# Optimization experiments

Measured on AMD Instinct MI355X. Metric: run time of the kernel, lower is better.

## Reference

```python
import jax, jax.numpy as jnp
import numpy as np

NUM_USERS = 100000
NUM_RATINGS = 5
EMBED_DIM = 64
ATT_DIM = 16
B, G, L, S = 16384, 8, 50, 32


def setup_inputs() -> dict:
    key = jax.random.key(0)
    ks = jax.random.split(key, 16)
    inp = {
        # forward args (int / bool constants)
        "nodes": jax.random.randint(ks[0], (B, G), 0, NUM_USERS),
        "history_u": jax.random.randint(ks[1], (B, L), 0, NUM_USERS),
        "history_r": jax.random.randint(ks[2], (B, L), 0, NUM_RATINGS),
        "history_mask": jax.random.randint(ks[3], (B, L), 0, 2).astype(bool).at[:, 0].set(True),
        "social_adj": jax.random.randint(ks[4], (B, S), 0, NUM_USERS),
        "social_mask": jax.random.randint(ks[5], (B, S), 0, 2).astype(bool).at[:, 0].set(True),
        # learned parameters
        "features": jax.random.normal(ks[6], (NUM_USERS, EMBED_DIM), jnp.float32) * 0.02,
        "r_embed": jax.random.normal(ks[7], (NUM_RATINGS, EMBED_DIM), jnp.float32) * 0.02,
        "wg1": jax.random.normal(ks[8], (EMBED_DIM, ATT_DIM), jnp.float32) / np.sqrt(EMBED_DIM),
        "bg1": jnp.zeros((ATT_DIM,), jnp.float32),
        "wg2": jax.random.normal(ks[9], (ATT_DIM, 1), jnp.float32) / np.sqrt(ATT_DIM),
        "bg2": jnp.zeros((1,), jnp.float32),
        "w1": jax.random.normal(ks[10], (2 * EMBED_DIM, EMBED_DIM), jnp.float32) / np.sqrt(2 * EMBED_DIM),
        "b1": jnp.zeros((EMBED_DIM,), jnp.float32),
    }
    return inp


def _masked_mean(x, mask):
    # x: [B, N, D], mask: [B, N] float -> [B, D]
    denom = jnp.maximum(mask.sum(axis=1, keepdims=True), 1.0)
    return (x * mask[..., None]).sum(axis=1) / denom


def reference(nodes, history_u, history_r, history_mask, social_adj, social_mask,
              features, r_embed, wg1, bg1, wg2, bg2, w1, b1):
    dt = features.dtype
    # --- Group_Embedding: attention pooling over member embeddings ---
    members = features[nodes]                              # [B, G, D] gather
    h = jnp.tanh(members @ wg1 + bg1)                      # [B, G, 16]
    logits = (h @ wg2 + bg2)[..., 0]                       # [B, G]
    alpha = jax.nn.softmax(logits, axis=-1)
    self_feats = jnp.einsum('bg,bgd->bd', alpha, members)  # [B, D]

    # --- aggregator: ragged history (item+rating) + social neighbor means ---
    hm = history_mask.astype(dt)
    hist = features[history_u] + r_embed[history_r]        # [B, L, D] gather
    hist_mean = _masked_mean(hist, hm)                     # [B, D]

    sm = social_mask.astype(dt)
    soc_mean = _masked_mean(features[social_adj], sm)      # [B, D]

    neigh_feats = 0.5 * (hist_mean + soc_mean)             # [B, D]

    # --- concat -> linear -> relu ---
    combined = jnp.concatenate([self_feats, neigh_feats], axis=1)  # [B, 2D]
    return jax.nn.relu(combined @ w1 + b1)                 # [B, D]
```

## Files before the change

kernel.cpp:

```cpp
#include <hip/hip_runtime.h>
#include <cstdint>
#include <cstddef>

#define NUSERS 100000
#define BB 16384

static __device__ __forceinline__ unsigned short f2bf(float x) {
    unsigned u = __float_as_uint(x);
    u += 0x7FFF + ((u >> 16) & 1);
    return (unsigned short)(u >> 16);
}
static __device__ __forceinline__ float4 bf4_to_f4(ushort4 h) {
    float4 r;
    r.x = __uint_as_float((unsigned)h.x << 16);
    r.y = __uint_as_float((unsigned)h.y << 16);
    r.z = __uint_as_float((unsigned)h.z << 16);
    r.w = __uint_as_float((unsigned)h.w << 16);
    return r;
}

__global__ __launch_bounds__(256) void k0_scores(
    const float* __restrict__ features, const float* __restrict__ wg1,
    const float* __restrict__ bg1, const float* __restrict__ wg2,
    const float* __restrict__ bg2, float* __restrict__ Q,
    unsigned short* __restrict__ fbf)
{
    __shared__ float frow[16 * 68];
    __shared__ float wg1t[16 * 68];
    const int tid = threadIdx.x;
    const int blk = blockIdx.x;

    const float4 v = ((const float4*)(features + (size_t)blk * 1024))[tid];
    {
        const int row = tid >> 4, q = tid & 15;
        *(float4*)&frow[row * 68 + q * 4] = v;
    }
    {
        const float4 w = ((const float4*)wg1)[tid];
        const int d = tid >> 2, k0 = (tid & 3) * 4;
        wg1t[(k0 + 0) * 68 + d] = w.x;
        wg1t[(k0 + 1) * 68 + d] = w.y;
        wg1t[(k0 + 2) * 68 + d] = w.z;
        wg1t[(k0 + 3) * 68 + d] = w.w;
    }
    {
        ushort4 o;
        o.x = f2bf(v.x); o.y = f2bf(v.y); o.z = f2bf(v.z); o.w = f2bf(v.w);
        *(ushort4*)(fbf + (size_t)blk * 1024 + tid * 4) = o;
    }
    __syncthreads();

    const int k = tid & 15, ul = tid >> 4;
    float x = bg1[k];
    #pragma unroll
    for (int d4 = 0; d4 < 16; ++d4) {
        const float4 f  = *(const float4*)&frow[ul * 68 + d4 * 4];
        const float4 wv = *(const float4*)&wg1t[k * 68 + d4 * 4];
        x += f.x * wv.x + f.y * wv.y + f.z * wv.z + f.w * wv.w;
    }
    float xx = fminf(fmaxf(x, -9.f), 9.f);
    float e2 = __expf(2.f * xx);
    float th = (e2 - 1.f) / (e2 + 1.f);
    float t = th * wg2[k];
    t += __shfl_xor(t, 1);
    t += __shfl_xor(t, 2);
    t += __shfl_xor(t, 4);
    t += __shfl_xor(t, 8);
    if (k == 0) Q[blk * 16 + ul] = t + bg2[0];
}

__global__ __launch_bounds__(256) void k1_fuse(
    const int* __restrict__ nodes, const int* __restrict__ hist_u,
    const int* __restrict__ hist_r, const int* __restrict__ hist_m,
    const int* __restrict__ soc_a, const int* __restrict__ soc_m,
    const unsigned short* __restrict__ fbf, const float* __restrict__ r_embed,
    const float* __restrict__ Q, const float* __restrict__ w1,
    const float* __restrict__ b1, float* __restrict__ out)
{
    __shared__ float wvbuf[4][128];

    const int tid  = threadIdx.x;
    const int lane = tid & 63;
    const int wv   = tid >> 6;
    const int e    = blockIdx.x * 4 + wv;
    const int sub  = lane & 15;
    const int grp  = lane >> 4;
    const char* fb = (const char*)fbf;

    int*   lc = (int*)&wvbuf[wv][0];
    float* cb = &wvbuf[wv][0];

    lc[lane] = 0;
    if (lane < 32) lc[64 + lane] = 0;

    int nd = (lane < 8) ? nodes[e * 8 + lane] : 0;
    int hu = 0, hr = 0, hmv = 0;
    if (lane < 50) {
        hu  = hist_u[e * 50 + lane];
        hr  = hist_r[e * 50 + lane];
        hmv = hist_m[e * 50 + lane];
    }
    int sa = 0, sk = 0;
    if (lane < 32) {
        sa = soc_a[e * 32 + lane];
        sk = soc_m[e * 32 + lane];
    }

    uint64_t hb = __ballot(hmv != 0);
    const int hc = (int)__popcll(hb);
    int hrank = (int)__popcll(hb & ((1ull << lane) - 1));

    uint64_t sbm = __ballot(sk != 0);
    const int scn = (int)__popcll(sbm);
    int srank = (int)__popcll(sbm & ((1ull << lane) - 1));

    const float hw = 0.5f / (float)hc;
    const float sw = 0.5f / (float)scn;
    const int   n  = hc + scn;

    if (hmv) lc[hrank] = hu << 7;
    if (sk)  lc[hc + srank] = sa << 7;

    const int c0 = (int)__popcll(__ballot(hmv && hr == 0));
    const int c1 = (int)__popcll(__ballot(hmv && hr == 1));
    const int c2 = (int)__popcll(__ballot(hmv && hr == 2));
    const int c3 = (int)__popcll(__ballot(hmv && hr == 3));
    const int c4 = (int)__popcll(__ballot(hmv && hr == 4));

    int pkA = lc[lane];
    int pkB = lc[64 + (lane & 31)];

    float sc = (lane < 8) ? Q[nd] : -1e30f;
    float mx = sc;
    mx = fmaxf(mx, __shfl_xor(mx, 1));
    mx = fmaxf(mx, __shfl_xor(mx, 2));
    mx = fmaxf(mx, __shfl_xor(mx, 4));
    float ex = __expf(sc - mx);
    float sm = ex;
    sm += __shfl_xor(sm, 1);
    sm += __shfl_xor(sm, 2);
    sm += __shfl_xor(sm, 4);
    float al = ex / sm;

    float4 sf4;
    {
        const float a0 = __shfl(al, grp);
        const int   u0 = __shfl(nd, grp);
        const float a1 = __shfl(al, 4 + grp);
        const int   u1 = __shfl(nd, 4 + grp);
        const float4 v0 = bf4_to_f4(*(const ushort4*)(fb + ((unsigned)u0 << 7) + sub * 8));
        const float4 v1 = bf4_to_f4(*(const ushort4*)(fb + ((unsigned)u1 << 7) + sub * 8));
        sf4.x = a0 * v0.x + a1 * v1.x;
        sf4.y = a0 * v0.y + a1 * v1.y;
        sf4.z = a0 * v0.z + a1 * v1.z;
        sf4.w = a0 * v0.w + a1 * v1.w;
    }

    float4 nb4 = {0.f, 0.f, 0.f, 0.f};
    for (int base = 0; base < n; base += 16) {
        #pragma unroll
        for (int j = 0; j < 4; ++j) {
            const int cbase = base + j * 4;
            int off;
            if (cbase < 64) off = __shfl(pkA, cbase + grp);
            else            off = __shfl(pkB, cbase - 64 + grp);
            const int idx = cbase + grp;
            const float w = (idx < hc) ? hw : ((idx < n) ? sw : 0.f);
            const float4 v = bf4_to_f4(*(const ushort4*)(fb + (unsigned)off + sub * 8));
            nb4.x += w * v.x; nb4.y += w * v.y;
            nb4.z += w * v.z; nb4.w += w * v.w;
        }
    }

#define XRED(v4)                                            \
    v4.x += __shfl_xor(v4.x, 16); v4.x += __shfl_xor(v4.x, 32); \
    v4.y += __shfl_xor(v4.y, 16); v4.y += __shfl_xor(v4.y, 32); \
    v4.z += __shfl_xor(v4.z, 16); v4.z += __shfl_xor(v4.z, 32); \
    v4.w += __shfl_xor(v4.w, 16); v4.w += __shfl_xor(v4.w, 32);
    XRED(sf4)
    XRED(nb4)
#undef XRED

    {
        const float4* re4p = (const float4*)r_embed;
        const float4 re0 = re4p[0 * 16 + sub];
        const float4 re1 = re4p[1 * 16 + sub];
        const float4 re2 = re4p[2 * 16 + sub];
        const float4 re3 = re4p[3 * 16 + sub];
        const float4 re4 = re4p[4 * 16 + sub];
        float f0 = hw * (float)c0, f1 = hw * (float)c1, f2 = hw * (float)c2,
              f3 = hw * (float)c3, f4 = hw * (float)c4;
        nb4.x += f0 * re0.x + f1 * re1.x + f2 * re2.x + f3 * re3.x + f4 * re4.x;
        nb4.y += f0 * re0.y + f1 * re1.y + f2 * re2.y + f3 * re3.y + f4 * re4.y;
        nb4.z += f0 * re0.z + f1 * re1.z + f2 * re2.z + f3 * re3.z + f4 * re4.z;
        nb4.w += f0 * re0.w + f1 * re1.w + f2 * re2.w + f3 * re3.w + f4 * re4.w;
    }

    if (grp == 0) *(float4*)&cb[sub * 4] = sf4;
    if (grp == 1) *(float4*)&cb[64 + sub * 4] = nb4;

    float4 p = {0.f, 0.f, 0.f, 0.f};
    #pragma unroll 8
    for (int j = 0; j < 32; ++j) {
        const float  c   = cb[j * 4 + grp];
        const float4 wv4 = *(const float4*)(w1 + (j * 4 + grp) * 64 + sub * 4);
        p.x += c * wv4.x;
        p.y += c * wv4.y;
        p.z += c * wv4.z;
        p.w += c * wv4.w;
    }
    p.x += __shfl_xor(p.x, 16); p.x += __shfl_xor(p.x, 32);
    p.y += __shfl_xor(p.y, 16); p.y += __shfl_xor(p.y, 32);
    p.z += __shfl_xor(p.z, 16); p.z += __shfl_xor(p.z, 32);
    p.w += __shfl_xor(p.w, 16); p.w += __shfl_xor(p.w, 32);
    if (grp == 0) {
        const float4 bv = *(const float4*)(b1 + sub * 4);
        float4 o;
        o.x = fmaxf(p.x + bv.x, 0.f);
        o.y = fmaxf(p.y + bv.y, 0.f);
        o.z = fmaxf(p.z + bv.z, 0.f);
        o.w = fmaxf(p.w + bv.w, 0.f);
        *(float4*)(out + (size_t)e * 64 + sub * 4) = o;
    }
}

extern "C" void kernel_launch(void* const* d_in, const int* in_sizes, int n_in,
                              void* d_out, int out_size, void* d_ws, size_t ws_size,
                              hipStream_t stream)
{
    const int*   nodes    = (const int*)d_in[0];
    const int*   hu       = (const int*)d_in[1];
    const int*   hr       = (const int*)d_in[2];
    const int*   hm       = (const int*)d_in[3];
    const int*   sa       = (const int*)d_in[4];
    const int*   smk      = (const int*)d_in[5];
    const float* features = (const float*)d_in[6];
    const float* r_embed  = (const float*)d_in[7];
    const float* wg1      = (const float*)d_in[8];
    const float* bg1      = (const float*)d_in[9];
    const float* wg2      = (const float*)d_in[10];
    const float* bg2      = (const float*)d_in[11];
    const float* w1       = (const float*)d_in[12];
    const float* b1       = (const float*)d_in[13];
    float* out = (float*)d_out;

    float*          Q   = (float*)d_ws;
    unsigned short* fbf = (unsigned short*)(Q + 131072);

    k0_scores<<<NUSERS / 16, 256, 0, stream>>>(features, wg1, bg1, wg2, bg2, Q, fbf);
    k1_fuse<<<BB / 4, 256, 0, stream>>>(nodes, hu, hr, hm, sa, smk,
                                        fbf, r_embed, Q, w1, b1, out);
}
```

Before: 138.5 us.

## Gather bf16 rows with 16-byte loads, 8 rows per wave per step

```diff
diff --git a/kernel.cpp b/kernel.cpp
--- a/kernel.cpp
+++ b/kernel.cpp
@@ -10,13 +10,16 @@
     u += 0x7FFF + ((u >> 16) & 1);
     return (unsigned short)(u >> 16);
 }
-static __device__ __forceinline__ float4 bf4_to_f4(ushort4 h) {
-    float4 r;
-    r.x = __uint_as_float((unsigned)h.x << 16);
-    r.y = __uint_as_float((unsigned)h.y << 16);
-    r.z = __uint_as_float((unsigned)h.z << 16);
-    r.w = __uint_as_float((unsigned)h.w << 16);
-    return r;
+
+static __device__ __forceinline__ void acc8(float* acc, uint4 q, float w) {
+    acc[0] += w * __uint_as_float(q.x << 16);
+    acc[1] += w * __uint_as_float(q.x & 0xffff0000u);
+    acc[2] += w * __uint_as_float(q.y << 16);
+    acc[3] += w * __uint_as_float(q.y & 0xffff0000u);
+    acc[4] += w * __uint_as_float(q.z << 16);
+    acc[5] += w * __uint_as_float(q.z & 0xffff0000u);
+    acc[6] += w * __uint_as_float(q.w << 16);
+    acc[7] += w * __uint_as_float(q.w & 0xffff0000u);
 }
 
 __global__ __launch_bounds__(256) void k0_scores(
@@ -85,6 +88,8 @@
     const int e    = blockIdx.x * 4 + wv;
     const int sub  = lane & 15;
     const int grp  = lane >> 4;
+    const int oct  = lane >> 3;
+    const int s8   = lane & 7;
     const char* fb = (const char*)fbf;
 
     int*   lc = (int*)&wvbuf[wv][0];
@@ -131,6 +136,31 @@
     int pkB = lc[64 + (lane & 31)];
 
     float sc = (lane < 8) ? Q[nd] : -1e30f;
+    const int um = __shfl(nd, oct);
+    const uint4 mq = *(const uint4*)(fb + ((unsigned)um << 7) + s8 * 16);
+
+    float nb[8] = {0.f, 0.f, 0.f, 0.f, 0.f, 0.f, 0.f, 0.f};
+    for (int base = 0; base < n; base += 32) {
+        const int b0 = base, b1_ = base + 8, b2 = base + 16, b3 = base + 24;
+        const int off0 = (b0  < 64) ? __shfl(pkA, b0  + oct) : __shfl(pkB, b0  - 64 + oct);
+        const int off1 = (b1_ < 64) ? __shfl(pkA, b1_ + oct) : __shfl(pkB, b1_ - 64 + oct);
+        const int off2 = (b2  < 64) ? __shfl(pkA, b2  + oct) : __shfl(pkB, b2  - 64 + oct);
+        const int off3 = (b3  < 64) ? __shfl(pkA, b3  + oct) : __shfl(pkB, b3  - 64 + oct);
+        const uint4 q0 = *(const uint4*)(fb + (unsigned)off0 + s8 * 16);
+        const uint4 q1 = *(const uint4*)(fb + (unsigned)off1 + s8 * 16);
+        const uint4 q2 = *(const uint4*)(fb + (unsigned)off2 + s8 * 16);
+        const uint4 q3 = *(const uint4*)(fb + (unsigned)off3 + s8 * 16);
+        const int i0 = b0 + oct, i1 = b1_ + oct, i2 = b2 + oct, i3 = b3 + oct;
+        const float w0 = (i0 < hc) ? hw : ((i0 < n) ? sw : 0.f);
+        const float w1q= (i1 < hc) ? hw : ((i1 < n) ? sw : 0.f);
+        const float w2 = (i2 < hc) ? hw : ((i2 < n) ? sw : 0.f);
+        const float w3 = (i3 < hc) ? hw : ((i3 < n) ? sw : 0.f);
+        acc8(nb, q0, w0);
+        acc8(nb, q1, w1q);
+        acc8(nb, q2, w2);
+        acc8(nb, q3, w3);
+    }
+
     float mx = sc;
     mx = fmaxf(mx, __shfl_xor(mx, 1));
     mx = fmaxf(mx, __shfl_xor(mx, 2));
@@ -142,62 +172,47 @@
     sm += __shfl_xor(sm, 4);
     float al = ex / sm;
 
-    float4 sf4;
-    {
-        const float a0 = __shfl(al, grp);
-        const int   u0 = __shfl(nd, grp);
-        const float a1 = __shfl(al, 4 + grp);
-        const int   u1 = __shfl(nd, 4 + grp);
-        const float4 v0 = bf4_to_f4(*(const ushort4*)(fb + ((unsigned)u0 << 7) + sub * 8));
-        const float4 v1 = bf4_to_f4(*(const ushort4*)(fb + ((unsigned)u1 << 7) + sub * 8));
-        sf4.x = a0 * v0.x + a1 * v1.x;
-        sf4.y = a0 * v0.y + a1 * v1.y;
-        sf4.z = a0 * v0.z + a1 * v1.z;
-        sf4.w = a0 * v0.w + a1 * v1.w;
-    }
-
-    float4 nb4 = {0.f, 0.f, 0.f, 0.f};
-    for (int base = 0; base < n; base += 16) {
-        #pragma unroll
-        for (int j = 0; j < 4; ++j) {
-            const int cbase = base + j * 4;
-            int off;
-            if (cbase < 64) off = __shfl(pkA, cbase + grp);
-            else            off = __shfl(pkB, cbase - 64 + grp);
-            const int idx = cbase + grp;
-            const float w = (idx < hc) ? hw : ((idx < n) ? sw : 0.f);
-            const float4 v = bf4_to_f4(*(const ushort4*)(fb + (unsigned)off + sub * 8));
-            nb4.x += w * v.x; nb4.y += w * v.y;
-            nb4.z += w * v.z; nb4.w += w * v.w;
-        }
-    }
-
-#define XRED(v4)                                            \
-    v4.x += __shfl_xor(v4.x, 16); v4.x += __shfl_xor(v4.x, 32); \
-    v4.y += __shfl_xor(v4.y, 16); v4.y += __shfl_xor(v4.y, 32); \
-    v4.z += __shfl_xor(v4.z, 16); v4.z += __shfl_xor(v4.z, 32); \
-    v4.w += __shfl_xor(v4.w, 16); v4.w += __shfl_xor(v4.w, 32);
-    XRED(sf4)
-    XRED(nb4)
-#undef XRED
-
-    {
-        const float4* re4p = (const float4*)r_embed;
-        const float4 re0 = re4p[0 * 16 + sub];
-        const float4 re1 = re4p[1 * 16 + sub];
-        const float4 re2 = re4p[2 * 16 + sub];
-        const float4 re3 = re4p[3 * 16 + sub];
-        const float4 re4 = re4p[4 * 16 + sub];
-        float f0 = hw * (float)c0, f1 = hw * (float)c1, f2 = hw * (float)c2,
-              f3 = hw * (float)c3, f4 = hw * (float)c4;
-        nb4.x += f0 * re0.x + f1 * re1.x + f2 * re2.x + f3 * re3.x + f4 * re4.x;
-        nb4.y += f0 * re0.y + f1 * re1.y + f2 * re2.y + f3 * re3.y + f4 * re4.y;
-        nb4.z += f0 * re0.z + f1 * re1.z + f2 * re2.z + f3 * re3.z + f4 * re4.z;
-        nb4.w += f0 * re0.w + f1 * re1.w + f2 * re2.w + f3 * re3.w + f4 * re4.w;
-    }
-
-    if (grp == 0) *(float4*)&cb[sub * 4] = sf4;
-    if (grp == 1) *(float4*)&cb[64 + sub * 4] = nb4;
+    const float am = __shfl(al, oct);
+    float sf[8] = {0.f, 0.f, 0.f, 0.f, 0.f, 0.f, 0.f, 0.f};
+    acc8(sf, mq, am);
+
+    #pragma unroll
+    for (int k = 0; k < 8; ++k) {
+        nb[k] += __shfl_xor(nb[k], 8);
+        nb[k] += __shfl_xor(nb[k], 16);
+        nb[k] += __shfl_xor(nb[k], 32);
+        sf[k] += __shfl_xor(sf[k], 8);
+        sf[k] += __shfl_xor(sf[k], 16);
+        sf[k] += __shfl_xor(sf[k], 32);
+    }
+
+    {
+        const float4* r4 = (const float4*)r_embed;
+        const int qa = s8 * 2;
+        const float4 a0 = r4[0 * 16 + qa], b0 = r4[0 * 16 + qa + 1];
+        const float4 a1 = r4[1 * 16 + qa], b1v = r4[1 * 16 + qa + 1];
+        const float4 a2 = r4[2 * 16 + qa], b2v = r4[2 * 16 + qa + 1];
+        const float4 a3 = r4[3 * 16 + qa], b3v = r4[3 * 16 + qa + 1];
+        const float4 a4 = r4[4 * 16 + qa], b4v = r4[4 * 16 + qa + 1];
+        const float f0 = hw * (float)c0, f1 = hw * (float)c1, f2 = hw * (float)c2,
+                    f3 = hw * (float)c3, f4 = hw * (float)c4;
+        nb[0] += f0 * a0.x + f1 * a1.x + f2 * a2.x + f3 * a3.x + f4 * a4.x;
+        nb[1] += f0 * a0.y + f1 * a1.y + f2 * a2.y + f3 * a3.y + f4 * a4.y;
+        nb[2] += f0 * a0.z + f1 * a1.z + f2 * a2.z + f3 * a3.z + f4 * a4.z;
+        nb[3] += f0 * a0.w + f1 * a1.w + f2 * a2.w + f3 * a3.w + f4 * a4.w;
+        nb[4] += f0 * b0.x + f1 * b1v.x + f2 * b2v.x + f3 * b3v.x + f4 * b4v.x;
+        nb[5] += f0 * b0.y + f1 * b1v.y + f2 * b2v.y + f3 * b3v.y + f4 * b4v.y;
+        nb[6] += f0 * b0.z + f1 * b1v.z + f2 * b2v.z + f3 * b3v.z + f4 * b4v.z;
+        nb[7] += f0 * b0.w + f1 * b1v.w + f2 * b2v.w + f3 * b3v.w + f4 * b4v.w;
+    }
+
+    if (oct == 0) {
+        *(float4*)&cb[s8 * 8]     = make_float4(sf[0], sf[1], sf[2], sf[3]);
+        *(float4*)&cb[s8 * 8 + 4] = make_float4(sf[4], sf[5], sf[6], sf[7]);
+    } else if (oct == 1) {
+        *(float4*)&cb[64 + s8 * 8]     = make_float4(nb[0], nb[1], nb[2], nb[3]);
+        *(float4*)&cb[64 + s8 * 8 + 4] = make_float4(nb[4], nb[5], nb[6], nb[7]);
+    }
 
     float4 p = {0.f, 0.f, 0.f, 0.f};
     #pragma unroll 8
```

After: 140.6 us. No clear change (+1.5%).

## Precompute per-user W1 projections with MFMA and gather projected rows

Applied to the files above, without the earlier changes.

```diff
diff --git a/kernel.cpp b/kernel.cpp
--- a/kernel.cpp
+++ b/kernel.cpp
@@ -4,80 +4,146 @@
 
 #define NUSERS 100000
 #define BB 16384
+
+typedef __attribute__((ext_vector_type(8))) short bf16x8;
+typedef __attribute__((ext_vector_type(4))) float f32x4;
 
 static __device__ __forceinline__ unsigned short f2bf(float x) {
     unsigned u = __float_as_uint(x);
     u += 0x7FFF + ((u >> 16) & 1);
     return (unsigned short)(u >> 16);
 }
-static __device__ __forceinline__ float4 bf4_to_f4(ushort4 h) {
-    float4 r;
-    r.x = __uint_as_float((unsigned)h.x << 16);
-    r.y = __uint_as_float((unsigned)h.y << 16);
-    r.z = __uint_as_float((unsigned)h.z << 16);
-    r.w = __uint_as_float((unsigned)h.w << 16);
-    return r;
-}
-
-__global__ __launch_bounds__(256) void k0_scores(
-    const float* __restrict__ features, const float* __restrict__ wg1,
-    const float* __restrict__ bg1, const float* __restrict__ wg2,
-    const float* __restrict__ bg2, float* __restrict__ Q,
-    unsigned short* __restrict__ fbf)
+static __device__ __forceinline__ float bf2f(unsigned short h) {
+    return __uint_as_float((unsigned)h << 16);
+}
+
+__global__ __launch_bounds__(256) void k0_build(
+    const float* __restrict__ features, const float* __restrict__ r_embed,
+    const float* __restrict__ wg1, const float* __restrict__ bg1,
+    const float* __restrict__ wg2, const float* __restrict__ bg2,
+    const float* __restrict__ w1,
+    float* __restrict__ Q, float* __restrict__ RB, float* __restrict__ GH)
 {
-    __shared__ float frow[16 * 68];
-    __shared__ float wg1t[16 * 68];
+    __shared__ unsigned short Al[64 * 72];
+    __shared__ unsigned short Bt[128 * 72];
+    __shared__ float wg1t[16 * 72];
+
     const int tid = threadIdx.x;
     const int blk = blockIdx.x;
-
-    const float4 v = ((const float4*)(features + (size_t)blk * 1024))[tid];
-    {
-        const int row = tid >> 4, q = tid & 15;
-        *(float4*)&frow[row * 68 + q * 4] = v;
+    const int u0  = blk * 64;
+
+    #pragma unroll
+    for (int q = 0; q < 4; ++q) {
+        const int idx = tid + q * 256;
+        const int ul  = idx >> 4, qd = idx & 15;
+        float4 v = make_float4(0.f, 0.f, 0.f, 0.f);
+        if (u0 + ul < NUSERS)
+            v = *(const float4*)(features + (size_t)(u0 + ul) * 64 + qd * 4);
+        ushort4 o;
+        o.x = f2bf(v.x); o.y = f2bf(v.y); o.z = f2bf(v.z); o.w = f2bf(v.w);
+        *(ushort4*)&Al[ul * 72 + qd * 4] = o;
+    }
+    #pragma unroll
+    for (int q = 0; q < 8; ++q) {
+        const int idx = tid + q * 256;
+        const int r  = idx >> 4, cq = (idx & 15) * 4;
+        const float4 v = *(const float4*)(w1 + r * 64 + cq);
+        const int cc = (r < 64) ? cq : (64 + cq);
+        const int dd = (r < 64) ? r : (r - 64);
+        Bt[(cc + 0) * 72 + dd] = f2bf(v.x);
+        Bt[(cc + 1) * 72 + dd] = f2bf(v.y);
+        Bt[(cc + 2) * 72 + dd] = f2bf(v.z);
+        Bt[(cc + 3) * 72 + dd] = f2bf(v.w);
     }
     {
         const float4 w = ((const float4*)wg1)[tid];
-        const int d = tid >> 2, k0 = (tid & 3) * 4;
-        wg1t[(k0 + 0) * 68 + d] = w.x;
-        wg1t[(k0 + 1) * 68 + d] = w.y;
-        wg1t[(k0 + 2) * 68 + d] = w.z;
-        wg1t[(k0 + 3) * 68 + d] = w.w;
-    }
+        const int d = tid >> 2, k0q = (tid & 3) * 4;
+        wg1t[(k0q + 0) * 72 + d] = w.x;
+        wg1t[(k0q + 1) * 72 + d] = w.y;
+        wg1t[(k0q + 2) * 72 + d] = w.z;
+        wg1t[(k0q + 3) * 72 + d] = w.w;
+    }
+    __syncthreads();
+
+    const int lane = tid & 63, wv = tid >> 6;
+    const int arow = wv * 16 + (lane & 15);
+    const int hi   = lane >> 4;
+    f32x4 acc[8];
+    #pragma unroll
+    for (int ct = 0; ct < 8; ++ct) acc[ct] = (f32x4){0.f, 0.f, 0.f, 0.f};
+    #pragma unroll
+    for (int ks = 0; ks < 2; ++ks) {
+        const bf16x8 a = *(const bf16x8*)&Al[arow * 72 + ks * 32 + hi * 8];
+        #pragma unroll
+        for (int ct = 0; ct < 8; ++ct) {
+            const bf16x8 b = *(const bf16x8*)&Bt[(ct * 16 + (lane & 15)) * 72 + ks * 32 + hi * 8];
+            acc[ct] = __builtin_amdgcn_mfma_f32_16x16x32_bf16(a, b, acc[ct], 0, 0, 0);
+        }
+    }
+    #pragma unroll
+    for (int ct = 0; ct < 8; ++ct) {
+        #pragma unroll
+        for (int j = 0; j < 4; ++j) {
+            const int ul = wv * 16 + hi * 4 + j;
+            const int u  = u0 + ul;
+            if (u < NUSERS)
+                GH[(size_t)u * 128 + ct * 16 + (lane & 15)] = acc[ct][j];
+        }
+    }
+
     {
-        ushort4 o;
-        o.x = f2bf(v.x); o.y = f2bf(v.y); o.z = f2bf(v.z); o.w = f2bf(v.w);
-        *(ushort4*)(fbf + (size_t)blk * 1024 + tid * 4) = o;
-    }
-    __syncthreads();
-
-    const int k = tid & 15, ul = tid >> 4;
-    float x = bg1[k];
-    #pragma unroll
-    for (int d4 = 0; d4 < 16; ++d4) {
-        const float4 f  = *(const float4*)&frow[ul * 68 + d4 * 4];
-        const float4 wv = *(const float4*)&wg1t[k * 68 + d4 * 4];
-        x += f.x * wv.x + f.y * wv.y + f.z * wv.z + f.w * wv.w;
-    }
-    float xx = fminf(fmaxf(x, -9.f), 9.f);
-    float e2 = __expf(2.f * xx);
-    float th = (e2 - 1.f) / (e2 + 1.f);
-    float t = th * wg2[k];
-    t += __shfl_xor(t, 1);
-    t += __shfl_xor(t, 2);
-    t += __shfl_xor(t, 4);
-    t += __shfl_xor(t, 8);
-    if (k == 0) Q[blk * 16 + ul] = t + bg2[0];
+        const int k = tid & 15, ug = tid >> 4;
+        const float bg1v = bg1[k], wk2 = wg2[k], bg2v = bg2[0];
+        #pragma unroll
+        for (int un = 0; un < 4; ++un) {
+            const int ul = ug + un * 16;
+            float x = bg1v;
+            #pragma unroll
+            for (int d8 = 0; d8 < 8; ++d8) {
+                const ushort4 pa = *(const ushort4*)&Al[ul * 72 + d8 * 8];
+                const ushort4 pb = *(const ushort4*)&Al[ul * 72 + d8 * 8 + 4];
+                x += bf2f(pa.x) * wg1t[k * 72 + d8 * 8 + 0]
+                   + bf2f(pa.y) * wg1t[k * 72 + d8 * 8 + 1]
+                   + bf2f(pa.z) * wg1t[k * 72 + d8 * 8 + 2]
+                   + bf2f(pa.w) * wg1t[k * 72 + d8 * 8 + 3]
+                   + bf2f(pb.x) * wg1t[k * 72 + d8 * 8 + 4]
+                   + bf2f(pb.y) * wg1t[k * 72 + d8 * 8 + 5]
+                   + bf2f(pb.z) * wg1t[k * 72 + d8 * 8 + 6]
+                   + bf2f(pb.w) * wg1t[k * 72 + d8 * 8 + 7];
+            }
+            float xx = fminf(fmaxf(x, -9.f), 9.f);
+            float e2 = __expf(2.f * xx);
+            float th = (e2 - 1.f) / (e2 + 1.f);
+            float t = th * wk2;
+            t += __shfl_xor(t, 1);
+            t += __shfl_xor(t, 2);
+            t += __shfl_xor(t, 4);
+            t += __shfl_xor(t, 8);
+            if (k == 0 && u0 + ul < NUSERS) Q[u0 + ul] = t + bg2v;
+        }
+    }
+
+    if (blk == 0) {
+        for (int t = tid; t < 320; t += 256) {
+            const int r = t >> 6, c = t & 63;
+            float a = 0.f;
+            #pragma unroll 8
+            for (int d = 0; d < 64; ++d)
+                a += r_embed[r * 64 + d] * w1[(64 + d) * 64 + c];
+            RB[r * 64 + c] = a;
+        }
+    }
 }
 
 __global__ __launch_bounds__(256) void k1_fuse(
     const int* __restrict__ nodes, const int* __restrict__ hist_u,
     const int* __restrict__ hist_r, const int* __restrict__ hist_m,
     const int* __restrict__ soc_a, const int* __restrict__ soc_m,
-    const unsigned short* __restrict__ fbf, const float* __restrict__ r_embed,
-    const float* __restrict__ Q, const float* __restrict__ w1,
-    const float* __restrict__ b1, float* __restrict__ out)
+    const float* __restrict__ GH, const float* __restrict__ RB,
+    const float* __restrict__ Q, const float* __restrict__ b1,
+    float* __restrict__ out)
 {
-    __shared__ float wvbuf[4][128];
+    __shared__ int lcomp[4][96];
 
     const int tid  = threadIdx.x;
     const int lane = tid & 63;
@@ -85,10 +151,9 @@
     const int e    = blockIdx.x * 4 + wv;
     const int sub  = lane & 15;
     const int grp  = lane >> 4;
-    const char* fb = (const char*)fbf;
-
-    int*   lc = (int*)&wvbuf[wv][0];
-    float* cb = &wvbuf[wv][0];
+    const char* fb = (const char*)GH;
+
+    int* lc = lcomp[wv];
 
     lc[lane] = 0;
     if (lane < 32) lc[64 + lane] = 0;
@@ -118,8 +183,8 @@
     const float sw = 0.5f / (float)scn;
     const int   n  = hc + scn;
 
-    if (hmv) lc[hrank] = hu << 7;
-    if (sk)  lc[hc + srank] = sa << 7;
+    if (hmv) lc[hrank] = (hu << 9) + 256;
+    if (sk)  lc[hc + srank] = (sa << 9) + 256;
 
     const int c0 = (int)__popcll(__ballot(hmv && hr == 0));
     const int c1 = (int)__popcll(__ballot(hmv && hr == 1));
@@ -148,8 +213,8 @@
         const int   u0 = __shfl(nd, grp);
         const float a1 = __shfl(al, 4 + grp);
         const int   u1 = __shfl(nd, 4 + grp);
-        const float4 v0 = bf4_to_f4(*(const ushort4*)(fb + ((unsigned)u0 << 7) + sub * 8));
-        const float4 v1 = bf4_to_f4(*(const ushort4*)(fb + ((unsigned)u1 << 7) + sub * 8));
+        const float4 v0 = *(const float4*)(fb + ((unsigned)u0 << 9) + sub * 16);
+        const float4 v1 = *(const float4*)(fb + ((unsigned)u1 << 9) + sub * 16);
         sf4.x = a0 * v0.x + a1 * v1.x;
         sf4.y = a0 * v0.y + a1 * v1.y;
         sf4.z = a0 * v0.z + a1 * v1.z;
@@ -166,7 +231,7 @@
             else            off = __shfl(pkB, cbase - 64 + grp);
             const int idx = cbase + grp;
             const float w = (idx < hc) ? hw : ((idx < n) ? sw : 0.f);
-            const float4 v = bf4_to_f4(*(const ushort4*)(fb + (unsigned)off + sub * 8));
+            const float4 v = *(const float4*)(fb + (unsigned)off + sub * 16);
             nb4.x += w * v.x; nb4.y += w * v.y;
             nb4.z += w * v.z; nb4.w += w * v.w;
         }
@@ -182,44 +247,27 @@
 #undef XRED
 
     {
-        const float4* re4p = (const float4*)r_embed;
-        const float4 re0 = re4p[0 * 16 + sub];
-        const float4 re1 = re4p[1 * 16 + sub];
-        const float4 re2 = re4p[2 * 16 + sub];
-        const float4 re3 = re4p[3 * 16 + sub];
-        const float4 re4 = re4p[4 * 16 + sub];
-        float f0 = hw * (float)c0, f1 = hw * (float)c1, f2 = hw * (float)c2,
-              f3 = hw * (float)c3, f4 = hw * (float)c4;
-        nb4.x += f0 * re0.x + f1 * re1.x + f2 * re2.x + f3 * re3.x + f4 * re4.x;
-        nb4.y += f0 * re0.y + f1 * re1.y + f2 * re2.y + f3 * re3.y + f4 * re4.y;
-        nb4.z += f0 * re0.z + f1 * re1.z + f2 * re2.z + f3 * re3.z + f4 * re4.z;
-        nb4.w += f0 * re0.w + f1 * re1.w + f2 * re2.w + f3 * re3.w + f4 * re4.w;
-    }
-
-    if (grp == 0) *(float4*)&cb[sub * 4] = sf4;
-    if (grp == 1) *(float4*)&cb[64 + sub * 4] = nb4;
-
-    float4 p = {0.f, 0.f, 0.f, 0.f};
-    #pragma unroll 8
-    for (int j = 0; j < 32; ++j) {
-        const float  c   = cb[j * 4 + grp];
-        const float4 wv4 = *(const float4*)(w1 + (j * 4 + grp) * 64 + sub * 4);
-        p.x += c * wv4.x;
-        p.y += c * wv4.y;
-        p.z += c * wv4.z;
-        p.w += c * wv4.w;
-    }
-    p.x += __shfl_xor(p.x, 16); p.x += __shfl_xor(p.x, 32);
-    p.y += __shfl_xor(p.y, 16); p.y += __shfl_xor(p.y, 32);
-    p.z += __shfl_xor(p.z, 16); p.z += __shfl_xor(p.z, 32);
-    p.w += __shfl_xor(p.w, 16); p.w += __shfl_xor(p.w, 32);
+        const float4* rb4 = (const float4*)RB;
+        const float4 r0 = rb4[0 * 16 + sub];
+        const float4 r1 = rb4[1 * 16 + sub];
+        const float4 r2 = rb4[2 * 16 + sub];
+        const float4 r3 = rb4[3 * 16 + sub];
+        const float4 r4 = rb4[4 * 16 + sub];
+        const float f0 = hw * (float)c0, f1 = hw * (float)c1, f2 = hw * (float)c2,
+                    f3 = hw * (float)c3, f4 = hw * (float)c4;
+        nb4.x += f0 * r0.x + f1 * r1.x + f2 * r2.x + f3 * r3.x + f4 * r4.x;
+        nb4.y += f0 * r0.y + f1 * r1.y + f2 * r2.y + f3 * r3.y + f4 * r4.y;
+        nb4.z += f0 * r0.z + f1 * r1.z + f2 * r2.z + f3 * r3.z + f4 * r4.z;
+        nb4.w += f0 * r0.w + f1 * r1.w + f2 * r2.w + f3 * r3.w + f4 * r4.w;
+    }
+
     if (grp == 0) {
         const float4 bv = *(const float4*)(b1 + sub * 4);
         float4 o;
-        o.x = fmaxf(p.x + bv.x, 0.f);
-        o.y = fmaxf(p.y + bv.y, 0.f);
-        o.z = fmaxf(p.z + bv.z, 0.f);
-        o.w = fmaxf(p.w + bv.w, 0.f);
+        o.x = fmaxf(sf4.x + nb4.x + bv.x, 0.f);
+        o.y = fmaxf(sf4.y + nb4.y + bv.y, 0.f);
+        o.z = fmaxf(sf4.z + nb4.z + bv.z, 0.f);
+        o.w = fmaxf(sf4.w + nb4.w + bv.w, 0.f);
         *(float4*)(out + (size_t)e * 64 + sub * 4) = o;
     }
 }
@@ -244,10 +292,12 @@
     const float* b1       = (const float*)d_in[13];
     float* out = (float*)d_out;
 
-    float*          Q   = (float*)d_ws;
-    unsigned short* fbf = (unsigned short*)(Q + 131072);
-
-    k0_scores<<<NUSERS / 16, 256, 0, stream>>>(features, wg1, bg1, wg2, bg2, Q, fbf);
+    float* Q  = (float*)d_ws;
+    float* RB = Q + 131072;
+    float* GH = RB + 512;
+
+    k0_build<<<(NUSERS + 63) / 64, 256, 0, stream>>>(
+        features, r_embed, wg1, bg1, wg2, bg2, w1, Q, RB, GH);
     k1_fuse<<<BB / 4, 256, 0, stream>>>(nodes, hu, hr, hm, sa, smk,
-                                        fbf, r_embed, Q, w1, b1, out);
-}
+                                        GH, RB, Q, b1, out);
+}
```

After: 149.9 us. +8.2%, slower.
